# Optimization experiments

Hardware: AMD Instinct MI355X
Metric: run time of the kernel (lower is better)

The kernel has to match this reference:

```python
import jax, jax.numpy as jnp
import numpy as np

EPS = 1e-5

def setup_inputs() -> dict:
    key = jax.random.key(0)
    kx, kw = jax.random.split(key)
    x = jax.random.normal(kx, (2, 4096, 4096), dtype=jnp.float32)
    weight = jax.random.normal(kw, (16384, 4096), dtype=jnp.float32) * 0.02
    return {"x": x, "weight": weight}

def reference(x, weight):
    # Weight quantization: ternary {-1,0,1} via global mean-abs scale.
    # Note: original _quantize_weights does NOT rescale by `scale` afterwards.
    w_scale = jnp.maximum(jnp.mean(jnp.abs(weight)), EPS)
    w_q = jnp.clip(jnp.round(weight / w_scale), -1.0, 1.0)
    # Activation scaling: per-token abs-max over feature dim.
    x_scale = jnp.maximum(jnp.max(jnp.abs(x), axis=-1, keepdims=True), EPS)
    x_scaled = x / x_scale
    # F.linear(x_scaled, w_q) = x_scaled @ w_q.T  -> [B, S, N]
    out = jnp.einsum('bsk,nk->bsn', x_scaled, w_q)
    return out * x_scale
```

## Files before the change

### kernel.cpp

```cpp
#include <hip/hip_runtime.h>
#include <hip/hip_bf16.h>
#include <cstdint>

#define AS1 __attribute__((address_space(1)))
#define AS3 __attribute__((address_space(3)))

typedef unsigned short u16;
typedef unsigned int u32;
typedef __bf16 bf16_t;
typedef bf16_t bf16x8 __attribute__((ext_vector_type(8)));
typedef float f32x4 __attribute__((ext_vector_type(4)));

static constexpr int M = 8192;
static constexpr int N = 16384;
static constexpr int K = 4096;
static constexpr int BM = 128, BN = 128, BK = 32;
static constexpr long long W_ELEMS = (long long)N * K;
static constexpr long long X_ELEMS = (long long)M * K;

__device__ __forceinline__ u16 f32_to_bf16_rne(float f) {
    u32 u = __float_as_uint(f);
    u += 0x7fffu + ((u >> 16) & 1u);
    return (u16)(u >> 16);
}

__global__ void wabs_sum_kernel(const float* __restrict__ w, double* __restrict__ out) {
    __shared__ double sred[256];
    const float4* w4 = (const float4*)w;
    const int n4 = (int)(W_ELEMS / 4);
    double s = 0.0;
    for (int i = blockIdx.x * blockDim.x + threadIdx.x; i < n4; i += gridDim.x * blockDim.x) {
        float4 v = w4[i];
        s += (double)fabsf(v.x) + (double)fabsf(v.y) + (double)fabsf(v.z) + (double)fabsf(v.w);
    }
    sred[threadIdx.x] = s;
    __syncthreads();
    for (int off = 128; off > 0; off >>= 1) {
        if ((int)threadIdx.x < off) sred[threadIdx.x] += sred[threadIdx.x + off];
        __syncthreads();
    }
    if (threadIdx.x == 0) atomicAdd(out, sred[0]);
}

__global__ void w_quant_kernel(const float4* __restrict__ w4, const double* __restrict__ wsum,
                               ushort4* __restrict__ wq) {
    const double scale = fmax(wsum[0] * (1.0 / 67108864.0), 1e-5);
    const double inv = 1.0 / scale;
    const int n4 = (int)(W_ELEMS / 4);
    for (int i = blockIdx.x * blockDim.x + threadIdx.x; i < n4; i += gridDim.x * blockDim.x) {
        float4 v = w4[i];
        float q0 = fminf(fmaxf((float)rint((double)v.x * inv), -1.f), 1.f);
        float q1 = fminf(fmaxf((float)rint((double)v.y * inv), -1.f), 1.f);
        float q2 = fminf(fmaxf((float)rint((double)v.z * inv), -1.f), 1.f);
        float q3 = fminf(fmaxf((float)rint((double)v.w * inv), -1.f), 1.f);
        ushort4 o;
        o.x = f32_to_bf16_rne(q0);
        o.y = f32_to_bf16_rne(q1);
        o.z = f32_to_bf16_rne(q2);
        o.w = f32_to_bf16_rne(q3);
        wq[i] = o;
    }
}

__global__ void x_conv_kernel(const float4* __restrict__ x4, ushort4* __restrict__ xb) {
    const int n4 = (int)(X_ELEMS / 4);
    for (int i = blockIdx.x * blockDim.x + threadIdx.x; i < n4; i += gridDim.x * blockDim.x) {
        float4 v = x4[i];
        ushort4 o;
        o.x = f32_to_bf16_rne(v.x);
        o.y = f32_to_bf16_rne(v.y);
        o.z = f32_to_bf16_rne(v.z);
        o.w = f32_to_bf16_rne(v.w);
        xb[i] = o;
    }
}

__device__ __forceinline__ void gld16(const void* gptr, const void* lptr) {
    __builtin_amdgcn_global_load_lds(
        (AS1 u32*)(uintptr_t)gptr,
        (AS3 u32*)(u32)(uintptr_t)lptr,
        16, 0, 0);
}

__global__ __launch_bounds__(256) void gemm_bt_kernel(const u16* __restrict__ A,
                                                      const u16* __restrict__ B,
                                                      float* __restrict__ C) {
    __shared__ __align__(16) u16 sA[BM * BK];
    __shared__ __align__(16) u16 sB[BN * BK];

    const int tid = threadIdx.x;
    const int wid = tid >> 6;
    const int lane = tid & 63;

    constexpr int GM = 4;
    constexpr int NT = N / BN;
    const int bid = blockIdx.x;
    const int band = bid / (GM * NT);
    const int r0 = bid % (GM * NT);
    const int m0 = (band * GM + (r0 % GM)) * BM;
    const int n0 = (r0 / GM) * BN;

    const int srow = tid >> 2;
    const int scb = tid & 3;
    const u16* gA0 = A + (size_t)(m0 + srow) * K + scb * 8;
    const u16* gA1 = gA0 + (size_t)64 * K;
    const u16* gB0 = B + (size_t)(n0 + srow) * K + scb * 8;
    const u16* gB1 = gB0 + (size_t)64 * K;
    const u16* lA0 = &sA[wid * 512];
    const u16* lA1 = &sA[2048 + wid * 512];
    const u16* lB0 = &sB[wid * 512];
    const u16* lB1 = &sB[2048 + wid * 512];

    const int wm = (wid & 1) * 64;
    const int wn = (wid >> 1) * 64;
    const int fr = lane & 15;
    const int fq = lane >> 4;

    f32x4 acc[4][4] = {};

    for (int k0 = 0; k0 < K; k0 += BK) {
        __syncthreads();
        gld16(gA0 + k0, lA0);
        gld16(gA1 + k0, lA1);
        gld16(gB0 + k0, lB0);
        gld16(gB1 + k0, lB1);
        __syncthreads();

        bf16x8 a[4], b[4];
#pragma unroll
        for (int mt = 0; mt < 4; ++mt)
            a[mt] = *(const bf16x8*)&sA[(wm + mt * 16 + fr) * BK + fq * 8];
#pragma unroll
        for (int nt = 0; nt < 4; ++nt)
            b[nt] = *(const bf16x8*)&sB[(wn + nt * 16 + fr) * BK + fq * 8];
#pragma unroll
        for (int mt = 0; mt < 4; ++mt)
#pragma unroll
            for (int nt = 0; nt < 4; ++nt)
                acc[mt][nt] = __builtin_amdgcn_mfma_f32_16x16x32_bf16(a[mt], b[nt], acc[mt][nt], 0, 0, 0);
    }

#pragma unroll
    for (int mt = 0; mt < 4; ++mt) {
#pragma unroll
        for (int i = 0; i < 4; ++i) {
            const size_t rrow = (size_t)(m0 + wm + mt * 16 + fq * 4 + i);
            float* Crow = C + rrow * N + n0 + wn + fr;
#pragma unroll
            for (int nt = 0; nt < 4; ++nt)
                Crow[nt * 16] = acc[mt][nt][i];
        }
    }
}

extern "C" void kernel_launch(void* const* d_in, const int* in_sizes, int n_in,
                              void* d_out, int out_size, void* d_ws, size_t ws_size,
                              hipStream_t stream) {
    const float* x = (const float*)d_in[0];
    const float* w = (const float*)d_in[1];
    float* out = (float*)d_out;

    char* ws = (char*)d_ws;
    double* wsum = (double*)ws;
    u16* wq = (u16*)(ws + 256);
    u16* xb = (u16*)(ws + 256 + (size_t)W_ELEMS * 2);

    hipMemsetAsync(wsum, 0, 64, stream);
    wabs_sum_kernel<<<1024, 256, 0, stream>>>(w, wsum);
    w_quant_kernel<<<4096, 256, 0, stream>>>((const float4*)w, wsum, (ushort4*)wq);
    x_conv_kernel<<<2048, 256, 0, stream>>>((const float4*)x, (ushort4*)xb);

    const int nblocks = (M / BM) * (N / BN);
    gemm_bt_kernel<<<nblocks, 256, 0, stream>>>(xb, wq, out);
}
```

Before: 2.746 ms.

## Double-buffer LDS tiles, use fragment-ordered LDS layout, and remap block ids

The GEMM kernel now keeps two LDS buffers per operand. It prefetches the next K tile while running MFMAs on the current one, which cuts the per-iteration barriers from two to one. The LDS tile is now stored in MFMA fragment order, so each lane reads 16 contiguous bytes, aiming to avoid bank conflicts and simplify addressing. Block ids are also permuted across the eight low bits, likely to group neighbouring tiles on the same XCD for L2 reuse. In exchange, LDS use doubles, and correctness relies on the barrier waiting for the async global-to-LDS loads.

```diff
diff --git a/kernel.cpp b/kernel.cpp
--- a/kernel.cpp
+++ b/kernel.cpp
@@ -85,59 +85,68 @@
 __global__ __launch_bounds__(256) void gemm_bt_kernel(const u16* __restrict__ A,
                                                       const u16* __restrict__ B,
                                                       float* __restrict__ C) {
-    __shared__ __align__(16) u16 sA[BM * BK];
-    __shared__ __align__(16) u16 sB[BN * BK];
+    __shared__ __align__(16) u16 sA[2][BM * BK];
+    __shared__ __align__(16) u16 sB[2][BN * BK];
 
     const int tid = threadIdx.x;
     const int wid = tid >> 6;
     const int lane = tid & 63;
+    const int fr = lane & 15;
+    const int fq = lane >> 4;
+
+    const int bid0 = blockIdx.x;
+    const int bid = ((bid0 & 7) << 10) | (bid0 >> 3);
 
     constexpr int GM = 4;
     constexpr int NT = N / BN;
-    const int bid = blockIdx.x;
     const int band = bid / (GM * NT);
     const int r0 = bid % (GM * NT);
     const int m0 = (band * GM + (r0 % GM)) * BM;
     const int n0 = (r0 / GM) * BN;
 
-    const int srow = tid >> 2;
-    const int scb = tid & 3;
-    const u16* gA0 = A + (size_t)(m0 + srow) * K + scb * 8;
+    const u16* gA0 = A + (size_t)(m0 + wid * 16 + fr) * K + fq * 8;
     const u16* gA1 = gA0 + (size_t)64 * K;
-    const u16* gB0 = B + (size_t)(n0 + srow) * K + scb * 8;
+    const u16* gB0 = B + (size_t)(n0 + wid * 16 + fr) * K + fq * 8;
     const u16* gB1 = gB0 + (size_t)64 * K;
-    const u16* lA0 = &sA[wid * 512];
-    const u16* lA1 = &sA[2048 + wid * 512];
-    const u16* lB0 = &sB[wid * 512];
-    const u16* lB1 = &sB[2048 + wid * 512];
 
     const int wm = (wid & 1) * 64;
     const int wn = (wid >> 1) * 64;
-    const int fr = lane & 15;
-    const int fq = lane >> 4;
+    const int ca = (wm >> 4) * 512;
+    const int cb = (wn >> 4) * 512;
 
     f32x4 acc[4][4] = {};
 
+    gld16(gA0, &sA[0][wid * 512]);
+    gld16(gA1, &sA[0][2048 + wid * 512]);
+    gld16(gB0, &sB[0][wid * 512]);
+    gld16(gB1, &sB[0][2048 + wid * 512]);
+    __syncthreads();
+
+    int cur = 0;
     for (int k0 = 0; k0 < K; k0 += BK) {
-        __syncthreads();
-        gld16(gA0 + k0, lA0);
-        gld16(gA1 + k0, lA1);
-        gld16(gB0 + k0, lB0);
-        gld16(gB1 + k0, lB1);
-        __syncthreads();
+        const int nxt = cur ^ 1;
+        if (k0 + BK < K) {
+            gld16(gA0 + k0 + BK, &sA[nxt][wid * 512]);
+            gld16(gA1 + k0 + BK, &sA[nxt][2048 + wid * 512]);
+            gld16(gB0 + k0 + BK, &sB[nxt][wid * 512]);
+            gld16(gB1 + k0 + BK, &sB[nxt][2048 + wid * 512]);
+        }
 
         bf16x8 a[4], b[4];
 #pragma unroll
         for (int mt = 0; mt < 4; ++mt)
-            a[mt] = *(const bf16x8*)&sA[(wm + mt * 16 + fr) * BK + fq * 8];
+            a[mt] = *(const bf16x8*)&sA[cur][ca + mt * 512 + lane * 8];
 #pragma unroll
         for (int nt = 0; nt < 4; ++nt)
-            b[nt] = *(const bf16x8*)&sB[(wn + nt * 16 + fr) * BK + fq * 8];
+            b[nt] = *(const bf16x8*)&sB[cur][cb + nt * 512 + lane * 8];
 #pragma unroll
         for (int mt = 0; mt < 4; ++mt)
 #pragma unroll
             for (int nt = 0; nt < 4; ++nt)
                 acc[mt][nt] = __builtin_amdgcn_mfma_f32_16x16x32_bf16(a[mt], b[nt], acc[mt][nt], 0, 0, 0);
+
+        __syncthreads();
+        cur = nxt;
     }
 
 #pragma unroll
```

Measured after the change: 2.670 ms. 2.8% less time.
